# Kernel optimization log

Measured on AMD Instinct MI355X. Metric: run time of the kernel, lower is better.

The kernel has to match this reference:

```python
import jax, jax.numpy as jnp
import numpy as np

V, D, L = 256, 512, 12
B, S = 8, 8192
EPS = 1e-5


def layernorm(x, g, b):
    mu = jnp.mean(x, axis=-1, keepdims=True)
    var = jnp.var(x, axis=-1, keepdims=True)
    return (x - mu) * jax.lax.rsqrt(var + EPS) * g + b


def log_g(x):
    # log of g(x) = x+0.5 if x>=0 else sigmoid(x)
    return jnp.where(x >= 0, jnp.log(jax.nn.relu(x) + 0.5), -jax.nn.softplus(-x))


def heinsen_scan_log(log_coeffs, log_values):
    # h_t = a_t * h_{t-1} + b_t in log-space, parallel over seq (axis=1)
    a_star = jnp.cumsum(log_coeffs, axis=1)
    log_h0_plus_b = jax.lax.cumlogsumexp(log_values - a_star, axis=1)
    return jnp.exp(a_star + log_h0_plus_b)


def min_gru(x, W):
    hg = x @ W                      # [B,S,2D]
    hidden, gate = hg[..., :D], hg[..., D:]
    log_coeffs = -jax.nn.softplus(gate)      # log(1 - z)
    log_z = -jax.nn.softplus(-gate)          # log z
    log_values = log_z + log_g(hidden)
    return heinsen_scan_log(log_coeffs, log_values)


def setup_inputs() -> dict:
    key = jax.random.key(0)
    k0, k1, k2 = jax.random.split(key, 3)
    tokens = jax.random.randint(k0, (B, S), 0, V)
    emb = jax.random.normal(k1, (V, D), dtype=jnp.float32) * 0.02
    # xavier uniform for Linear(D, 2D): fan_in=D, fan_out=2D
    lim = float(np.sqrt(6.0 / (D + 2 * D)))
    W = jax.random.uniform(k2, (L, D, 2 * D), minval=-lim, maxval=lim, dtype=jnp.float32)
    return {
        "tokens": tokens,
        "emb": emb,
        "ln_g": jnp.ones((L, D), jnp.float32),
        "ln_b": jnp.zeros((L, D), jnp.float32),
        "W": W,
        "norm_g": jnp.ones((D,), jnp.float32),
        "norm_b": jnp.zeros((D,), jnp.float32),
    }


def reference(tokens, emb, ln_g, ln_b, W, norm_g, norm_b):
    x = emb[tokens]                 # [B,S,D]
    for i in range(L):
        h = layernorm(x, ln_g[i], ln_b[i])
        x = x + min_gru(h, W[i])
    x = layernorm(x, norm_g, norm_b)
    logits = x @ emb.T              # tied lm_head, [B,S,V]
    return logits
```

## Files before the change

kernel.cpp:

```cpp
#include <hip/hip_runtime.h>
#include <stdint.h>

#define D 512
#define VOCAB 256
#define NLAYER 12
#define BB 8
#define SS 8192
#define CH 128
#define SL 64

typedef __bf16 bf16x8 __attribute__((ext_vector_type(8)));
typedef float f32x4 __attribute__((ext_vector_type(4)));
typedef _Float16 half2_t __attribute__((ext_vector_type(2)));

__device__ __forceinline__ unsigned short f2bf(float f) {
  union { float f; uint32_t u; } c; c.f = f;
  uint32_t u = c.u;
  u += 0x7FFFu + ((u >> 16) & 1u);
  return (unsigned short)(u >> 16);
}

__device__ __forceinline__ void st_f32(float* p, float v) { *p = v; }
__device__ __forceinline__ void st_f32(unsigned short* p, float v) { *p = f2bf(v); }

__device__ __forceinline__ float rcpf_(float x) { return __builtin_amdgcn_rcpf(x); }

__device__ __forceinline__ uint32_t pack_fv(float f, float v) {
  union { half2_t h; uint32_t u; } c;
  c.h.x = (_Float16)f;
  c.h.y = (_Float16)v;
  return c.u;
}

__device__ __forceinline__ void unpack_fv(uint32_t u, float& f, float& v) {
  union { uint32_t u; half2_t h; } c; c.u = u;
  f = (float)c.h.x;
  v = (float)c.h.y;
}

__device__ __forceinline__ void gl_lds16(const unsigned short* g, unsigned short* l) {
  __builtin_amdgcn_global_load_lds((const __attribute__((address_space(1))) void*)(const void*)g,
                                   (__attribute__((address_space(3))) void*)(void*)l, 16, 0, 0);
}

__global__ __launch_bounds__(256) void k_gather(const int* __restrict__ toks,
                                                const float* __restrict__ emb,
                                                float* __restrict__ x) {
  int T = blockIdx.x * 256 + threadIdx.x;
  int row = T >> 6, lane = T & 63;
  int tok = toks[row] & (VOCAB - 1);
  const float4* s = (const float4*)(emb + (size_t)tok * D) + lane * 2;
  float4* d = (float4*)(x + (size_t)row * D) + lane * 2;
  d[0] = s[0];
  d[1] = s[1];
}

__global__ __launch_bounds__(256) void k_convW(const float* __restrict__ W,
                                               unsigned short* __restrict__ Wt) {
  __shared__ float tile[32][33];
  int bid = blockIdx.x;
  int l = bid >> 9;
  int rem = bid & 511;
  int kt = rem >> 5, nt = rem & 31;
  int k0 = kt * 32, n0 = nt * 32;
  int tx = threadIdx.x & 31, ty = threadIdx.x >> 5;
  const float* Wl = W + (size_t)l * D * 2 * D;
  for (int i = 0; i < 4; i++) {
    int k = k0 + ty + 8 * i;
    tile[ty + 8 * i][tx] = Wl[(size_t)k * 1024 + n0 + tx];
  }
  __syncthreads();
  unsigned short* Wtl = Wt + (size_t)l * 1024 * D;
  for (int i = 0; i < 4; i++) {
    int n = n0 + ty + 8 * i;
    Wtl[(size_t)n * D + k0 + tx] = f2bf(tile[tx][ty + 8 * i]);
  }
}

__global__ __launch_bounds__(256) void k_fragW(const unsigned short* __restrict__ Wt,
                                               unsigned short* __restrict__ WtF) {
  int t = blockIdx.x * 256 + threadIdx.x;
  int lane = t & 63;
  int tile = t >> 6;
  int l = tile >> 10;
  int rem = tile & 1023;
  int n16 = rem >> 4, kt = rem & 15;
  const unsigned short* src = Wt + (size_t)l * 1024 * 512 +
                              (size_t)(n16 * 16 + (lane & 15)) * 512 + kt * 32 + (lane >> 4) * 8;
  unsigned short* dst = WtF + (size_t)l * 1024 * 512 + ((size_t)tile * 64 + lane) * 8 -
                        (size_t)l * 1024 * 512 + (size_t)l * 1024 * 512;
  *(uint4*)(WtF + (size_t)l * 524288 + ((size_t)rem * 64 + lane) * 8) = *(const uint4*)src;
  (void)dst;
}

__global__ __launch_bounds__(256) void k_convEmb(const float* __restrict__ e,
                                                 unsigned short* __restrict__ o) {
  int t = blockIdx.x * 256 + threadIdx.x;
  const float4* s = (const float4*)e + (size_t)t * 2;
  float4 a = s[0], b = s[1];
  uint32_t w0 = (uint32_t)f2bf(a.x) | ((uint32_t)f2bf(a.y) << 16);
  uint32_t w1 = (uint32_t)f2bf(a.z) | ((uint32_t)f2bf(a.w) << 16);
  uint32_t w2 = (uint32_t)f2bf(b.x) | ((uint32_t)f2bf(b.y) << 16);
  uint32_t w3 = (uint32_t)f2bf(b.z) | ((uint32_t)f2bf(b.w) << 16);
  uint4 r; r.x = w0; r.y = w1; r.z = w2; r.w = w3;
  ((uint4*)o)[t] = r;
}

__global__ __launch_bounds__(256) void k_ln(const float* __restrict__ x,
                                            const float* __restrict__ g,
                                            const float* __restrict__ b,
                                            unsigned short* __restrict__ o) {
  int wv = threadIdx.x >> 6, lane = threadIdx.x & 63;
  size_t row = (size_t)blockIdx.x * 4 + wv;
  const float4* xr = (const float4*)(x + row * D) + lane * 2;
  float4 v0 = xr[0], v1 = xr[1];
  float s = v0.x + v0.y + v0.z + v0.w + v1.x + v1.y + v1.z + v1.w;
  float ss = v0.x * v0.x + v0.y * v0.y + v0.z * v0.z + v0.w * v0.w +
             v1.x * v1.x + v1.y * v1.y + v1.z * v1.z + v1.w * v1.w;
  for (int m = 32; m; m >>= 1) {
    s += __shfl_xor(s, m, 64);
    ss += __shfl_xor(ss, m, 64);
  }
  float mu = s * (1.0f / 512.0f);
  float var = ss * (1.0f / 512.0f) - mu * mu;
  float rstd = rsqrtf(var + 1e-5f);
  const float4* gp = (const float4*)g + lane * 2;
  const float4* bp = (const float4*)b + lane * 2;
  float4 g0 = gp[0], g1 = gp[1], b0 = bp[0], b1 = bp[1];
  uint32_t w0 = (uint32_t)f2bf((v0.x - mu) * rstd * g0.x + b0.x) |
                ((uint32_t)f2bf((v0.y - mu) * rstd * g0.y + b0.y) << 16);
  uint32_t w1 = (uint32_t)f2bf((v0.z - mu) * rstd * g0.z + b0.z) |
                ((uint32_t)f2bf((v0.w - mu) * rstd * g0.w + b0.w) << 16);
  uint32_t w2 = (uint32_t)f2bf((v1.x - mu) * rstd * g1.x + b1.x) |
                ((uint32_t)f2bf((v1.y - mu) * rstd * g1.y + b1.y) << 16);
  uint32_t w3 = (uint32_t)f2bf((v1.z - mu) * rstd * g1.z + b1.z) |
                ((uint32_t)f2bf((v1.w - mu) * rstd * g1.w + b1.w) << 16);
  uint4 r; r.x = w0; r.y = w1; r.z = w2; r.w = w3;
  ((uint4*)(o + row * D))[lane] = r;
}

__global__ __launch_bounds__(256, 2) void k_gemm_act(const unsigned short* __restrict__ A,
                                                     const unsigned short* __restrict__ Bt,
                                                     uint32_t* __restrict__ fv,
                                                     float* __restrict__ P,
                                                     float* __restrict__ Q) {
  __shared__ __align__(16) unsigned short As[64 * 512];
  const int tid = threadIdx.x;
  const int lane = tid & 63;
  const int wave = tid >> 6;
  const int m0 = blockIdx.x * 64;
  const int qm = lane & 15;
  const int hi = lane >> 4;
  for (int j = 0; j < 16; j++) {
    int r = wave * 16 + j;
    int cg = (lane & ~7) | ((lane & 7) ^ (r & 7));
    gl_lds16(A + (size_t)(m0 + r) * 512 + cg * 8, As + r * 512);
  }
  __syncthreads();

  const int b_loc = m0 >> 13;
  const int c_chunk = (m0 & (SS - 1)) >> 6;
  const size_t pq0 = ((size_t)b_loc * CH + c_chunk) * 512;

  for (int np = 0; np < 2; np++) {
    const int c0 = np * 256 + wave * 64;
    const int n16h = (c0 >> 4);
    f32x4 ah[4][4] = {};
    f32x4 ag[4][4] = {};
    bf16x8 bh[2][4], bg[2][4];
    for (int j = 0; j < 4; j++) {
      bh[0][j] = *(const bf16x8*)(Bt + (((size_t)(n16h + j) * 16 + 0) * 64 + lane) * 8);
      bg[0][j] = *(const bf16x8*)(Bt + (((size_t)(n16h + j + 32) * 16 + 0) * 64 + lane) * 8);
    }
    for (int kt = 0; kt < 16; kt++) {
      const int cur = kt & 1;
      if (kt < 15) {
        const int nxt = cur ^ 1;
        for (int j = 0; j < 4; j++) {
          bh[nxt][j] = *(const bf16x8*)(Bt + (((size_t)(n16h + j) * 16 + kt + 1) * 64 + lane) * 8);
          bg[nxt][j] = *(const bf16x8*)(Bt + (((size_t)(n16h + j + 32) * 16 + kt + 1) * 64 + lane) * 8);
        }
      }
      bf16x8 af[4];
      for (int i = 0; i < 4; i++) {
        int row = i * 16 + qm;
        int cgd = kt * 4 + hi;
        int cl = (cgd & ~7) | ((cgd & 7) ^ (row & 7));
        af[i] = *(const bf16x8*)(&As[row * 512 + cl * 8]);
      }
      for (int i = 0; i < 4; i++)
        for (int j = 0; j < 4; j++) {
          ah[i][j] = __builtin_amdgcn_mfma_f32_16x16x32_bf16(af[i], bh[cur][j], ah[i][j], 0, 0, 0);
          ag[i][j] = __builtin_amdgcn_mfma_f32_16x16x32_bf16(af[i], bg[cur][j], ag[i][j], 0, 0, 0);
        }
    }
    const int rq = hi * 4;
    for (int j = 0; j < 4; j++) {
      float cp = 1.f, cq = 0.f;
      for (int i = 0; i < 4; i++) {
        float sp = 1.f, sq = 0.f;
        for (int r = 0; r < 4; r++) {
          float h = ah[i][j][r];
          float g = ag[i][j][r];
          float e = __expf(g);
          float f = rcpf_(1.0f + e);
          float sg = 1.0f - f;
          float gf = h >= 0.0f ? h + 0.5f : rcpf_(1.0f + __expf(-h));
          float v = sg * gf;
          int rowg = m0 + i * 16 + rq + r;
          fv[(size_t)rowg * 512 + c0 + j * 16 + qm] = pack_fv(f, v);
          sp *= f;
          sq = sq * f + v;
        }
        float op = __shfl_xor(sp, 16), oq = __shfl_xor(sq, 16);
        float tp = sp * op;
        float tq = (lane & 16) ? (oq * sp + sq) : (sq * op + oq);
        op = __shfl_xor(tp, 32); oq = __shfl_xor(tq, 32);
        sp = tp * op;
        sq = (lane & 32) ? (oq * tp + tq) : (tq * op + oq);
        cq = cq * sp + sq;
        cp = cp * sp;
      }
      if (hi == 0) {
        P[pq0 + c0 + j * 16 + qm] = cp;
        Q[pq0 + c0 + j * 16 + qm] = cq;
      }
    }
  }
}

__global__ __launch_bounds__(256) void k_gemm(const unsigned short* __restrict__ A,
                                              const unsigned short* __restrict__ Bt,
                                              float* __restrict__ C, int N, int MT) {
  __shared__ __align__(16) unsigned short As[128 * 64];
  __shared__ __align__(16) unsigned short Bs[128 * 64];
  const int tid = threadIdx.x;
  const int lane = tid & 63;
  const int wave = tid >> 6;
  const int bid = blockIdx.x;
  const int mt = bid % MT;
  const int nt = bid / MT;
  const int m0 = mt * 128, n0 = nt * 128;
  const int wr = (wave >> 1) * 64;
  const int wc = (wave & 1) * 64;
  const int lrow = lane >> 3;
  const int lcs = ((lane & 7) ^ lrow) * 8;
  const unsigned short* Ag = A + (size_t)(m0 + wave * 32 + lrow) * 512 + lcs;
  const unsigned short* Bg = Bt + (size_t)(n0 + wave * 32 + lrow) * 512 + lcs;
  unsigned short* Al = As + wave * 32 * 64;
  unsigned short* Bl = Bs + wave * 32 * 64;
  const int qm = lane & 15;
  const int hi = lane >> 4;
  f32x4 acc[4][4] = {};
  for (int k0 = 0; k0 < 512; k0 += 64) {
    for (int j = 0; j < 4; j++) gl_lds16(Ag + k0 + (size_t)j * 8 * 512, Al + j * 512);
    for (int j = 0; j < 4; j++) gl_lds16(Bg + k0 + (size_t)j * 8 * 512, Bl + j * 512);
    __syncthreads();
    for (int ks = 0; ks < 2; ks++) {
      const int sw = ((ks * 4 + hi) ^ (qm & 7)) * 8;
      bf16x8 af[4], bfr[4];
      for (int i = 0; i < 4; i++) {
        af[i] = *(const bf16x8*)(&As[(wr + i * 16 + qm) * 64 + sw]);
        bfr[i] = *(const bf16x8*)(&Bs[(wc + i * 16 + qm) * 64 + sw]);
      }
      for (int i = 0; i < 4; i++)
        for (int j = 0; j < 4; j++)
          acc[i][j] = __builtin_amdgcn_mfma_f32_16x16x32_bf16(af[i], bfr[j], acc[i][j], 0, 0, 0);
    }
    __syncthreads();
  }
  const int col = lane & 15;
  const int rq = (lane >> 4) * 4;
  for (int i = 0; i < 4; i++)
    for (int j = 0; j < 4; j++)
      for (int r = 0; r < 4; r++)
        C[(size_t)(m0 + wr + i * 16 + rq + r) * N + (n0 + wc + j * 16 + col)] = acc[i][j][r];
}

__global__ __launch_bounds__(256) void k_scan2(const float* __restrict__ P,
                                               const float* __restrict__ Q,
                                               float* __restrict__ Hs) {
  int T = blockIdx.x * 256 + threadIdx.x;
  int d = T & 511;
  int b = T >> 9;
  float h = 0.f;
  for (int c = 0; c < CH; c++) {
    size_t i = ((size_t)b * CH + c) * 512 + d;
    Hs[i] = h;
    h = P[i] * h + Q[i];
  }
}

__global__ __launch_bounds__(256) void k_scan3(const uint32_t* __restrict__ fv,
                                               const float* __restrict__ Hs,
                                               float* __restrict__ x) {
  int T = blockIdx.x * 256 + threadIdx.x;
  int d = T & 511;
  int bc = T >> 9;
  int c = bc & (CH - 1);
  int b = bc >> 7;
  const uint32_t* base = fv + ((size_t)b * SS + c * SL) * 512 + d;
  float* xb = x + ((size_t)b * SS + c * SL) * 512 + d;
  float h = Hs[T];
  for (int s = 0; s < SL; s++) {
    float f, v;
    unpack_fv(base[(size_t)s * 512], f, v);
    h = f * h + v;
    xb[(size_t)s * 512] += h;
  }
}

extern "C" void kernel_launch(void* const* d_in, const int* in_sizes, int n_in,
                              void* d_out, int out_size, void* d_ws, size_t ws_size,
                              hipStream_t stream) {
  const int* toks = (const int*)d_in[0];
  const float* emb = (const float*)d_in[1];
  const float* ln_g = (const float*)d_in[2];
  const float* ln_b = (const float*)d_in[3];
  const float* W = (const float*)d_in[4];
  const float* norm_g = (const float*)d_in[5];
  const float* norm_b = (const float*)d_in[6];
  float* out = (float*)d_out;

  const int gbs[4] = {8, 4, 2, 1};
  int GB = 1;
  for (int i = 0; i < 4; i++) {
    size_t MGv = (size_t)gbs[i] * SS;
    size_t need = MGv * 5120 + 2 * 12582912 + 262144 + (size_t)gbs[i] * 786432;
    if (need <= ws_size) { GB = gbs[i]; break; }
  }
  const int MG = GB * SS;
  const int MT128 = MG / 128;

  char* p = (char*)d_ws;
  float* x = (float*)p;                     p += (size_t)MG * 2048;
  uint32_t* fv = (uint32_t*)p;              p += (size_t)MG * 2048;
  unsigned short* hbf = (unsigned short*)p; p += (size_t)MG * 1024;
  unsigned short* Wtrow = (unsigned short*)p; p += 12582912;
  unsigned short* WtF = (unsigned short*)p;   p += 12582912;
  unsigned short* ebf = (unsigned short*)p;   p += 262144;
  float* P = (float*)p;                     p += (size_t)GB * 262144;
  float* Q = (float*)p;                     p += (size_t)GB * 262144;
  float* Hs = (float*)p;

  k_convW<<<NLAYER * 512, 256, 0, stream>>>(W, Wtrow);
  k_fragW<<<NLAYER * 1024 * 64 / 256, 256, 0, stream>>>(Wtrow, WtF);
  k_convEmb<<<64, 256, 0, stream>>>(emb, ebf);

  for (int g = 0; g < BB / GB; g++) {
    const int* tg = toks + (size_t)g * MG;
    float* outg = out + (size_t)g * MG * VOCAB;

    k_gather<<<MG / 4, 256, 0, stream>>>(tg, emb, x);
    for (int l = 0; l < NLAYER; l++) {
      k_ln<<<MG / 4, 256, 0, stream>>>(x, ln_g + l * D, ln_b + l * D, hbf);
      k_gemm_act<<<MG / 64, 256, 0, stream>>>(hbf, WtF + (size_t)l * 524288, fv, P, Q);
      k_scan2<<<GB * 2, 256, 0, stream>>>(P, Q, Hs);
      k_scan3<<<GB * CH * 2, 256, 0, stream>>>(fv, Hs, x);
    }
    k_ln<<<MG / 4, 256, 0, stream>>>(x, norm_g, norm_b, hbf);
    k_gemm<<<2 * MT128, 256, 0, stream>>>(hbf, ebf, outg, VOCAB, MT128);
  }
}
```

Baseline: 3.129 ms.

## Halve scan chunk length and pre-fragment A tile in LDS for GEMM

```diff
diff --git a/kernel.cpp b/kernel.cpp
--- a/kernel.cpp
+++ b/kernel.cpp
@@ -6,8 +6,8 @@
 #define NLAYER 12
 #define BB 8
 #define SS 8192
-#define CH 128
-#define SL 64
+#define CH 256
+#define SL 32
 
 typedef __bf16 bf16x8 __attribute__((ext_vector_type(8)));
 typedef float f32x4 __attribute__((ext_vector_type(4)));
@@ -19,9 +19,6 @@
   u += 0x7FFFu + ((u >> 16) & 1u);
   return (unsigned short)(u >> 16);
 }
-
-__device__ __forceinline__ void st_f32(float* p, float v) { *p = v; }
-__device__ __forceinline__ void st_f32(unsigned short* p, float v) { *p = f2bf(v); }
 
 __device__ __forceinline__ float rcpf_(float x) { return __builtin_amdgcn_rcpf(x); }
 
@@ -85,12 +82,9 @@
   int l = tile >> 10;
   int rem = tile & 1023;
   int n16 = rem >> 4, kt = rem & 15;
-  const unsigned short* src = Wt + (size_t)l * 1024 * 512 +
+  const unsigned short* src = Wt + (size_t)l * 524288 +
                               (size_t)(n16 * 16 + (lane & 15)) * 512 + kt * 32 + (lane >> 4) * 8;
-  unsigned short* dst = WtF + (size_t)l * 1024 * 512 + ((size_t)tile * 64 + lane) * 8 -
-                        (size_t)l * 1024 * 512 + (size_t)l * 1024 * 512;
   *(uint4*)(WtF + (size_t)l * 524288 + ((size_t)rem * 64 + lane) * 8) = *(const uint4*)src;
-  (void)dst;
 }
 
 __global__ __launch_bounds__(256) void k_convEmb(const float* __restrict__ e,
@@ -151,79 +145,82 @@
   const int m0 = blockIdx.x * 64;
   const int qm = lane & 15;
   const int hi = lane >> 4;
+
   for (int j = 0; j < 16; j++) {
-    int r = wave * 16 + j;
-    int cg = (lane & ~7) | ((lane & 7) ^ (r & 7));
-    gl_lds16(A + (size_t)(m0 + r) * 512 + cg * 8, As + r * 512);
+    int T = wave * 16 + j;
+    int i = T & 3, kt = T >> 2;
+    gl_lds16(A + (size_t)(m0 + i * 16 + qm) * 512 + kt * 32 + hi * 8,
+             As + (size_t)T * 512);
   }
   __syncthreads();
 
   const int b_loc = m0 >> 13;
-  const int c_chunk = (m0 & (SS - 1)) >> 6;
-  const size_t pq0 = ((size_t)b_loc * CH + c_chunk) * 512;
+  const int c2 = (m0 & (SS - 1)) >> 5;
+  const size_t pqA = ((size_t)b_loc * CH + c2) * 512;
+  const size_t pqB = ((size_t)b_loc * CH + c2 + 1) * 512;
 
   for (int np = 0; np < 2; np++) {
     const int c0 = np * 256 + wave * 64;
-    const int n16h = (c0 >> 4);
-    f32x4 ah[4][4] = {};
-    f32x4 ag[4][4] = {};
-    bf16x8 bh[2][4], bg[2][4];
-    for (int j = 0; j < 4; j++) {
-      bh[0][j] = *(const bf16x8*)(Bt + (((size_t)(n16h + j) * 16 + 0) * 64 + lane) * 8);
-      bg[0][j] = *(const bf16x8*)(Bt + (((size_t)(n16h + j + 32) * 16 + 0) * 64 + lane) * 8);
-    }
-    for (int kt = 0; kt < 16; kt++) {
-      const int cur = kt & 1;
-      if (kt < 15) {
-        const int nxt = cur ^ 1;
-        for (int j = 0; j < 4; j++) {
-          bh[nxt][j] = *(const bf16x8*)(Bt + (((size_t)(n16h + j) * 16 + kt + 1) * 64 + lane) * 8);
-          bg[nxt][j] = *(const bf16x8*)(Bt + (((size_t)(n16h + j + 32) * 16 + kt + 1) * 64 + lane) * 8);
+    for (int jp = 0; jp < 2; jp++) {
+      const int n16 = (c0 >> 4) + jp * 2;
+      f32x4 ah[4][2] = {};
+      f32x4 ag[4][2] = {};
+      bf16x8 bh[2][2], bg[2][2];
+      for (int j = 0; j < 2; j++) {
+        bh[0][j] = *(const bf16x8*)(Bt + (((size_t)(n16 + j) * 16 + 0) * 64 + lane) * 8);
+        bg[0][j] = *(const bf16x8*)(Bt + (((size_t)(n16 + j + 32) * 16 + 0) * 64 + lane) * 8);
+      }
+      for (int kt = 0; kt < 16; kt++) {
+        const int cur = kt & 1;
+        if (kt < 15) {
+          const int nxt = cur ^ 1;
+          for (int j = 0; j < 2; j++) {
+            bh[nxt][j] = *(const bf16x8*)(Bt + (((size_t)(n16 + j) * 16 + kt + 1) * 64 + lane) * 8);
+            bg[nxt][j] = *(const bf16x8*)(Bt + (((size_t)(n16 + j + 32) * 16 + kt + 1) * 64 + lane) * 8);
+          }
         }
+        bf16x8 af[4];
+        for (int i = 0; i < 4; i++)
+          af[i] = *(const bf16x8*)(&As[((size_t)(kt * 4 + i)) * 512 + lane * 8]);
+        for (int i = 0; i < 4; i++)
+          for (int j = 0; j < 2; j++) {
+            ah[i][j] = __builtin_amdgcn_mfma_f32_16x16x32_bf16(af[i], bh[cur][j], ah[i][j], 0, 0, 0);
+            ag[i][j] = __builtin_amdgcn_mfma_f32_16x16x32_bf16(af[i], bg[cur][j], ag[i][j], 0, 0, 0);
+          }
       }
-      bf16x8 af[4];
-      for (int i = 0; i < 4; i++) {
-        int row = i * 16 + qm;
-        int cgd = kt * 4 + hi;
-        int cl = (cgd & ~7) | ((cgd & 7) ^ (row & 7));
-        af[i] = *(const bf16x8*)(&As[row * 512 + cl * 8]);
-      }
-      for (int i = 0; i < 4; i++)
-        for (int j = 0; j < 4; j++) {
-          ah[i][j] = __builtin_amdgcn_mfma_f32_16x16x32_bf16(af[i], bh[cur][j], ah[i][j], 0, 0, 0);
-          ag[i][j] = __builtin_amdgcn_mfma_f32_16x16x32_bf16(af[i], bg[cur][j], ag[i][j], 0, 0, 0);
+      for (int j = 0; j < 2; j++) {
+        const int colg = c0 + (jp * 2 + j) * 16 + qm;
+        float cp0 = 1.f, cq0 = 0.f, cp1 = 1.f, cq1 = 0.f;
+        for (int i = 0; i < 4; i++) {
+          float sp = 1.f, sq = 0.f;
+          for (int r = 0; r < 4; r++) {
+            float h = ah[i][j][r];
+            float g = ag[i][j][r];
+            float e = __expf(g);
+            float f = rcpf_(1.0f + e);
+            float sg = 1.0f - f;
+            float gf = h >= 0.0f ? h + 0.5f : rcpf_(1.0f + __expf(-h));
+            float v = sg * gf;
+            int rowg = m0 + i * 16 + hi * 4 + r;
+            fv[(size_t)rowg * 512 + colg] = pack_fv(f, v);
+            sp *= f;
+            sq = sq * f + v;
+          }
+          float op = __shfl_xor(sp, 16), oq = __shfl_xor(sq, 16);
+          float tp = sp * op;
+          float tq = (lane & 16) ? (oq * sp + sq) : (sq * op + oq);
+          op = __shfl_xor(tp, 32); oq = __shfl_xor(tq, 32);
+          sp = tp * op;
+          sq = (lane & 32) ? (oq * tp + tq) : (tq * op + oq);
+          if (i < 2) { cq0 = cq0 * sp + sq; cp0 *= sp; }
+          else       { cq1 = cq1 * sp + sq; cp1 *= sp; }
         }
-    }
-    const int rq = hi * 4;
-    for (int j = 0; j < 4; j++) {
-      float cp = 1.f, cq = 0.f;
-      for (int i = 0; i < 4; i++) {
-        float sp = 1.f, sq = 0.f;
-        for (int r = 0; r < 4; r++) {
-          float h = ah[i][j][r];
-          float g = ag[i][j][r];
-          float e = __expf(g);
-          float f = rcpf_(1.0f + e);
-          float sg = 1.0f - f;
-          float gf = h >= 0.0f ? h + 0.5f : rcpf_(1.0f + __expf(-h));
-          float v = sg * gf;
-          int rowg = m0 + i * 16 + rq + r;
-          fv[(size_t)rowg * 512 + c0 + j * 16 + qm] = pack_fv(f, v);
-          sp *= f;
-          sq = sq * f + v;
+        if (hi == 0) {
+          P[pqA + colg] = cp0;
+          Q[pqA + colg] = cq0;
+          P[pqB + colg] = cp1;
+          Q[pqB + colg] = cq1;
         }
-        float op = __shfl_xor(sp, 16), oq = __shfl_xor(sq, 16);
-        float tp = sp * op;
-        float tq = (lane & 16) ? (oq * sp + sq) : (sq * op + oq);
-        op = __shfl_xor(tp, 32); oq = __shfl_xor(tq, 32);
-        sp = tp * op;
-        sq = (lane & 32) ? (oq * tp + tq) : (tq * op + oq);
-        cq = cq * sp + sq;
-        cp = cp * sp;
-      }
-      if (hi == 0) {
-        P[pq0 + c0 + j * 16 + qm] = cp;
-        Q[pq0 + c0 + j * 16 + qm] = cq;
       }
     }
   }
@@ -298,10 +295,10 @@
   int d = T & 511;
   int bc = T >> 9;
   int c = bc & (CH - 1);
-  int b = bc >> 7;
+  int b = bc >> 8;
   const uint32_t* base = fv + ((size_t)b * SS + c * SL) * 512 + d;
   float* xb = x + ((size_t)b * SS + c * SL) * 512 + d;
-  float h = Hs[T];
+  float h = Hs[(size_t)bc * 512 + d];
   for (int s = 0; s < SL; s++) {
     float f, v;
     unpack_fv(base[(size_t)s * 512], f, v);
@@ -326,21 +323,21 @@
   int GB = 1;
   for (int i = 0; i < 4; i++) {
     size_t MGv = (size_t)gbs[i] * SS;
-    size_t need = MGv * 5120 + 2 * 12582912 + 262144 + (size_t)gbs[i] * 786432;
+    size_t need = MGv * 5120 + 2 * 12582912 + 262144 + (size_t)gbs[i] * 3 * 524288;
     if (need <= ws_size) { GB = gbs[i]; break; }
   }
   const int MG = GB * SS;
   const int MT128 = MG / 128;
 
   char* p = (char*)d_ws;
-  float* x = (float*)p;                     p += (size_t)MG * 2048;
-  uint32_t* fv = (uint32_t*)p;              p += (size_t)MG * 2048;
-  unsigned short* hbf = (unsigned short*)p; p += (size_t)MG * 1024;
+  float* x = (float*)p;                       p += (size_t)MG * 2048;
+  uint32_t* fv = (uint32_t*)p;                p += (size_t)MG * 2048;
+  unsigned short* hbf = (unsigned short*)p;   p += (size_t)MG * 1024;
   unsigned short* Wtrow = (unsigned short*)p; p += 12582912;
   unsigned short* WtF = (unsigned short*)p;   p += 12582912;
   unsigned short* ebf = (unsigned short*)p;   p += 262144;
-  float* P = (float*)p;                     p += (size_t)GB * 262144;
-  float* Q = (float*)p;                     p += (size_t)GB * 262144;
+  float* P = (float*)p;                       p += (size_t)GB * 524288;
+  float* Q = (float*)p;                       p += (size_t)GB * 524288;
   float* Hs = (float*)p;
 
   k_convW<<<NLAYER * 512, 256, 0, stream>>>(W, Wtrow);
@@ -356,7 +353,7 @@
       k_ln<<<MG / 4, 256, 0, stream>>>(x, ln_g + l * D, ln_b + l * D, hbf);
       k_gemm_act<<<MG / 64, 256, 0, stream>>>(hbf, WtF + (size_t)l * 524288, fv, P, Q);
       k_scan2<<<GB * 2, 256, 0, stream>>>(P, Q, Hs);
-      k_scan3<<<GB * CH * 2, 256, 0, stream>>>(fv, Hs, x);
+      k_scan3<<<GB * 512, 256, 0, stream>>>(fv, Hs, x);
     }
     k_ln<<<MG / 4, 256, 0, stream>>>(x, norm_g, norm_b, hbf);
     k_gemm<<<2 * MT128, 256, 0, stream>>>(hbf, ebf, outg, VOCAB, MT128);
```

Measured after the change: 5.462 ms. 74.6% more time.
